# Kernel tuning notes

Measured on AMD Instinct MI355X. Metric: run time of the kernel, lower is better.

Reference implementation:

```python
import jax, jax.numpy as jnp
import numpy as np

N_NODES = 50000
N_EDGES = 640000
D = 128
L = 3


def setup_inputs() -> dict:
    key = jax.random.key(0)
    k1, k2, k3, k4 = jax.random.split(key, 4)
    x = jax.random.normal(k1, (N_NODES, D), dtype=jnp.float32)
    # Glorot-ish scale so activations stay O(1) across 3 layers
    Ws = jax.random.normal(k2, (L, D, D), dtype=jnp.float32) * (1.0 / np.sqrt(D))
    bs = jnp.zeros((L, D), dtype=jnp.float32)
    edge_src = jax.random.randint(k3, (N_EDGES,), 0, N_NODES, dtype=jnp.int32)
    edge_dst = jax.random.randint(k4, (N_EDGES,), 0, N_NODES, dtype=jnp.int32)
    return {"x": x, "Ws": Ws, "bs": bs, "edge_src": edge_src, "edge_dst": edge_dst}


def reference(x, Ws, bs, edge_src, edge_dst):
    n = x.shape[0]
    ones = jnp.ones(edge_src.shape[0], dtype=x.dtype)
    # degrees, clamped to 1 as in dgl GraphConv(norm='both')
    deg_out = jnp.maximum(jax.ops.segment_sum(ones, edge_src, num_segments=n), 1.0)
    deg_in = jnp.maximum(jax.ops.segment_sum(ones, edge_dst, num_segments=n), 1.0)
    inv_sqrt_out = jax.lax.rsqrt(deg_out)[:, None]  # [N,1]
    inv_sqrt_in = jax.lax.rsqrt(deg_in)[:, None]    # [N,1]
    for l in range(Ws.shape[0]):
        h = x * inv_sqrt_out                         # src normalization
        msg = h[edge_src]                            # [E,D] gather
        agg = jax.ops.segment_sum(msg, edge_dst, num_segments=n)  # [N,D] scatter-add
        h = agg * inv_sqrt_in                        # dst normalization
        x = jax.nn.relu(h @ Ws[l] + bs[l])           # linear + ReLU
    return x
```

## Files before the change

kernel.cpp:

```cpp
#include <hip/hip_runtime.h>
#include <hip/hip_fp16.h>

typedef __attribute__((ext_vector_type(8))) _Float16 half8;
typedef __attribute__((ext_vector_type(4))) float f32x4;
typedef unsigned int u32;
typedef unsigned short u16;

#define ELL_PAD 64
#define NCHUNK 64
#define RSZ 8192


__global__ __launch_bounds__(256) void hist2(const int* __restrict__ esrc,
                                             const int* __restrict__ edst,
                                             u32* __restrict__ psrc,
                                             u32* __restrict__ pdst,
                                             const float* __restrict__ Ws,
                                             _Float16* __restrict__ Whi,
                                             _Float16* __restrict__ Wlo,
                                             int E, int N, int chunk, int R,
                                             int histBlocks, int packTotal) {
  __shared__ u32 bs_[RSZ];
  __shared__ u32 bd_[RSZ];
  if (blockIdx.x >= histBlocks) {
    int i = (blockIdx.x - histBlocks) * 256 + threadIdx.x;
    if (i < packTotal) {
      int lane  = i & 63;
      int kstep = (i >> 6) & 3;
      int ntile = (i >> 8) & 7;
      int layer = i >> 11;
      int n  = ntile * 16 + (lane & 15);
      int k0 = kstep * 32 + (lane >> 4) * 8;
      const float* W = Ws + (size_t)layer * 128 * 128;
      size_t base = (size_t)i * 8;
      for (int j = 0; j < 8; j++) {
        float v = W[(k0 + j) * 128 + n];
        _Float16 hi = (_Float16)v;
        Whi[base + j] = hi;
        Wlo[base + j] = (_Float16)(v - (float)hi);
      }
    }
    return;
  }
  int c = blockIdx.x / R;
  int r = blockIdx.x % R;
  int base = r * RSZ;
  int hi = min(RSZ, N - base);
  if (hi <= 0) return;
  for (int j = threadIdx.x; j < RSZ; j += 256) { bs_[j] = 0; bd_[j] = 0; }
  __syncthreads();
  int e0 = c * chunk;
  int e1 = min(E, e0 + chunk);
  for (int i = e0 + threadIdx.x; i < e1; i += 256) {
    unsigned ls = (unsigned)(esrc[i] - base);
    unsigned ld = (unsigned)(edst[i] - base);
    if (ls < (unsigned)RSZ) atomicAdd(&bs_[ls], 1u);
    if (ld < (unsigned)RSZ) atomicAdd(&bd_[ld], 1u);
  }
  __syncthreads();
  u32* ds = psrc + (size_t)c * N + base;
  u32* dd = pdst + (size_t)c * N + base;
  for (int j = threadIdx.x; j < hi; j += 256) { ds[j] = bs_[j]; dd[j] = bd_[j]; }
}


__global__ __launch_bounds__(256) void prep(const u32* __restrict__ psrc,
                                            u32* __restrict__ pdst,
                                            int* __restrict__ deg_out,
                                            int* __restrict__ deg_in, int N) {
  int i = blockIdx.x * 256 + threadIdx.x;
  if (i >= N) return;
  u32 s0 = 0, s1 = 0, s2 = 0, s3 = 0;
#pragma unroll
  for (int c = 0; c < NCHUNK; c += 4) {
    s0 += psrc[(size_t)(c + 0) * N + i];
    s1 += psrc[(size_t)(c + 1) * N + i];
    s2 += psrc[(size_t)(c + 2) * N + i];
    s3 += psrc[(size_t)(c + 3) * N + i];
  }
  deg_out[i] = (int)(s0 + s1 + s2 + s3);
  u32 cnt[NCHUNK];
#pragma unroll
  for (int c = 0; c < NCHUNK; c++) cnt[c] = pdst[(size_t)c * N + i];
  u32 run = (u32)i * ELL_PAD;
#pragma unroll
  for (int c = 0; c < NCHUNK; c++) { u32 t = cnt[c]; cnt[c] = run; run += t; }
#pragma unroll
  for (int c = 0; c < NCHUNK; c++) pdst[(size_t)c * N + i] = cnt[c];
  deg_in[i] = (int)(run - (u32)i * ELL_PAD);
}


__global__ __launch_bounds__(256) void xscale(const float* __restrict__ x,
                                              const int* __restrict__ deg_out,
                                              __half2* __restrict__ xh, int n64) {
  int gid = blockIdx.x * 256 + threadIdx.x;
  if (gid >= n64) return;
  int row = gid >> 6;
  int d = deg_out[row]; if (d < 1) d = 1;
  float s = rsqrtf((float)d);
  float2 v = ((const float2*)x)[gid];
  xh[gid] = __floats2half2_rn(v.x * s, v.y * s);
}


__global__ __launch_bounds__(256) void place(const int* __restrict__ esrc,
                                             const int* __restrict__ edst,
                                             const u32* __restrict__ pdst,
                                             u16* __restrict__ ell,
                                             int E, int N, int chunk, int R) {
  __shared__ u32 cur[RSZ];
  int c = blockIdx.x / R;
  int r = blockIdx.x % R;
  int base = r * RSZ;
  int hi = min(RSZ, N - base);
  if (hi <= 0) return;
  for (int j = threadIdx.x; j < hi; j += 256)
    cur[j] = pdst[(size_t)c * N + base + j];
  __syncthreads();
  int e0 = c * chunk;
  int e1 = min(E, e0 + chunk);
  for (int i = e0 + threadIdx.x; i < e1; i += 256) {
    int d = edst[i];
    unsigned loc = (unsigned)(d - base);
    if (loc < (unsigned)hi) {
      u32 p = atomicAdd(&cur[loc], 1u);
      u32 idx = p - (u32)d * ELL_PAD;
      if (idx < ELL_PAD) ell[p] = (u16)esrc[i];
    }
  }
}


__global__ __launch_bounds__(512) void layer16(const __half2* __restrict__ xh,
                                               const int* __restrict__ deg_in,
                                               const u16* __restrict__ ell,
                                               const _Float16* __restrict__ Whi,
                                               const _Float16* __restrict__ Wlo,
                                               const float* __restrict__ bias,
                                               const int* __restrict__ deg_out,
                                               __half* __restrict__ out16,
                                               float* __restrict__ out32, int n) {
  __shared__ _Float16 As[16 * 136];
  const int wave = threadIdx.x >> 6;
  const int lane = threadIdx.x & 63;
  const int rowBase = blockIdx.x * 16;

  {
    int r0 = rowBase + wave * 2, r1 = r0 + 1;
    int d0 = (r0 < n) ? deg_in[r0] : 0;
    int d1 = (r1 < n) ? deg_in[r1] : 0;
    int l0 = d0 > ELL_PAD ? ELL_PAD : d0;
    int l1 = d1 > ELL_PAD ? ELL_PAD : d1;
    const u16* ep0 = ell + (size_t)(r0 < n ? r0 : 0) * ELL_PAD;
    const u16* ep1 = ell + (size_t)(r1 < n ? r1 : 0) * ELL_PAD;
    float ax0 = 0.f, ay0 = 0.f, ax1 = 0.f, ay1 = 0.f;

    int m = (l0 < l1 ? l0 : l1) & ~3;
    int e = 0;
    for (; e < m; e += 4) {
      ushort4 ia = *(const ushort4*)&ep0[e];
      ushort4 ib = *(const ushort4*)&ep1[e];
      __half2 a0 = xh[(size_t)ia.x * 64 + lane];
      __half2 a1 = xh[(size_t)ia.y * 64 + lane];
      __half2 a2 = xh[(size_t)ia.z * 64 + lane];
      __half2 a3 = xh[(size_t)ia.w * 64 + lane];
      __half2 b0 = xh[(size_t)ib.x * 64 + lane];
      __half2 b1 = xh[(size_t)ib.y * 64 + lane];
      __half2 b2 = xh[(size_t)ib.z * 64 + lane];
      __half2 b3 = xh[(size_t)ib.w * 64 + lane];
      float2 u0 = __half22float2(a0), u1 = __half22float2(a1);
      float2 u2 = __half22float2(a2), u3 = __half22float2(a3);
      float2 w0 = __half22float2(b0), w1 = __half22float2(b1);
      float2 w2 = __half22float2(b2), w3 = __half22float2(b3);
      ax0 += (u0.x + u1.x) + (u2.x + u3.x);
      ay0 += (u0.y + u1.y) + (u2.y + u3.y);
      ax1 += (w0.x + w1.x) + (w2.x + w3.x);
      ay1 += (w0.y + w1.y) + (w2.y + w3.y);
    }
    int e0i = e;
    for (; e0i + 4 <= l0; e0i += 4) {
      ushort4 ia = *(const ushort4*)&ep0[e0i];
      __half2 a0 = xh[(size_t)ia.x * 64 + lane];
      __half2 a1 = xh[(size_t)ia.y * 64 + lane];
      __half2 a2 = xh[(size_t)ia.z * 64 + lane];
      __half2 a3 = xh[(size_t)ia.w * 64 + lane];
      float2 u0 = __half22float2(a0), u1 = __half22float2(a1);
      float2 u2 = __half22float2(a2), u3 = __half22float2(a3);
      ax0 += (u0.x + u1.x) + (u2.x + u3.x);
      ay0 += (u0.y + u1.y) + (u2.y + u3.y);
    }
    for (; e0i < l0; e0i++) {
      float2 v = __half22float2(xh[(size_t)ep0[e0i] * 64 + lane]);
      ax0 += v.x; ay0 += v.y;
    }
    int e1i = e;
    for (; e1i + 4 <= l1; e1i += 4) {
      ushort4 ib = *(const ushort4*)&ep1[e1i];
      __half2 b0 = xh[(size_t)ib.x * 64 + lane];
      __half2 b1 = xh[(size_t)ib.y * 64 + lane];
      __half2 b2 = xh[(size_t)ib.z * 64 + lane];
      __half2 b3 = xh[(size_t)ib.w * 64 + lane];
      float2 w0 = __half22float2(b0), w1 = __half22float2(b1);
      float2 w2 = __half22float2(b2), w3 = __half22float2(b3);
      ax1 += (w0.x + w1.x) + (w2.x + w3.x);
      ay1 += (w0.y + w1.y) + (w2.y + w3.y);
    }
    for (; e1i < l1; e1i++) {
      float2 v = __half22float2(xh[(size_t)ep1[e1i] * 64 + lane]);
      ax1 += v.x; ay1 += v.y;
    }

    float si0 = rsqrtf((float)(d0 < 1 ? 1 : d0));
    float si1 = rsqrtf((float)(d1 < 1 ? 1 : d1));
    *(__half2*)&As[(size_t)(wave * 2 + 0) * 136 + lane * 2] =
        __floats2half2_rn(ax0 * si0, ay0 * si0);
    *(__half2*)&As[(size_t)(wave * 2 + 1) * 136 + lane * 2] =
        __floats2half2_rn(ax1 * si1, ay1 * si1);
  }
  __syncthreads();

  const int quad = lane >> 4;
  const int l16  = lane & 15;
  f32x4 acc = (f32x4){0.f, 0.f, 0.f, 0.f};
#pragma unroll
  for (int ks = 0; ks < 4; ks++) {
    half8 a = *(const half8*)&As[(size_t)l16 * 136 + ks * 32 + quad * 8];
    half8 bh = *(const half8*)&Whi[((wave * 4 + ks) * 64 + lane) * 8];
    half8 bl = *(const half8*)&Wlo[((wave * 4 + ks) * 64 + lane) * 8];
    acc = __builtin_amdgcn_mfma_f32_16x16x32_f16(a, bh, acc, 0, 0, 0);
    acc = __builtin_amdgcn_mfma_f32_16x16x32_f16(a, bl, acc, 0, 0, 0);
  }

  const int r0 = rowBase + quad * 4;
  const int col = wave * 16 + l16;
  const float bv = bias[col];
#pragma unroll
  for (int r = 0; r < 4; r++) {
    int row = r0 + r;
    if (row < n) {
      float v = fmaxf(acc[r] + bv, 0.f);
      if (out16) {
        int d = deg_out[row]; if (d < 1) d = 1;
        out16[(size_t)row * 128 + col] = __float2half(v * rsqrtf((float)d));
      } else {
        out32[(size_t)row * 128 + col] = v;
      }
    }
  }
}


extern "C" void kernel_launch(void* const* d_in, const int* in_sizes, int n_in,
                              void* d_out, int out_size, void* d_ws, size_t ws_size,
                              hipStream_t stream) {
  const float* x   = (const float*)d_in[0];
  const float* Ws  = (const float*)d_in[1];
  const float* bs  = (const float*)d_in[2];
  const int* esrc  = (const int*)d_in[3];
  const int* edst  = (const int*)d_in[4];

  const int D = 128;
  const int N = in_sizes[0] / D;
  const int E = in_sizes[3];
  const int L = in_sizes[1] / (D * D);
  const int Npad = ((N + 15) / 16) * 16;
  const int chunk = (E + NCHUNK - 1) / NCHUNK;
  const int R = (N + RSZ - 1) / RSZ;
  const int histBlocks = NCHUNK * R;
  const int packTotal = L * 2048;
  const int packBlocks = (packTotal + 255) / 256;

  char* base = (char*)d_ws;
  size_t off = 0;
  auto alloc = [&](size_t bytes) {
    char* p = base + off;
    off = (off + bytes + 255) & ~(size_t)255;
    return p;
  };
  int*      deg_out = (int*)alloc((size_t)N * 4);
  int*      deg_in  = (int*)alloc((size_t)N * 4);
  u16*      ell     = (u16*)alloc((size_t)N * ELL_PAD * 2);
  _Float16* Whi     = (_Float16*)alloc((size_t)L * 16384 * 2);
  _Float16* Wlo     = (_Float16*)alloc((size_t)L * 16384 * 2);
  _Float16* xh0     = (_Float16*)alloc((size_t)Npad * 128 * 2);
  _Float16* xh1     = (_Float16*)alloc((size_t)Npad * 128 * 2);
  u32*      psrc    = (u32*)alloc((size_t)NCHUNK * N * 4);
  u32*      pdst    = (u32*)alloc((size_t)NCHUNK * N * 4);

  hist2<<<dim3(histBlocks + packBlocks), dim3(256), 0, stream>>>(
      esrc, edst, psrc, pdst, Ws, Whi, Wlo, E, N, chunk, R, histBlocks, packTotal);
  prep<<<dim3((N + 255) / 256), dim3(256), 0, stream>>>(psrc, pdst, deg_out, deg_in, N);
  xscale<<<dim3((N * 64 + 255) / 256), dim3(256), 0, stream>>>(
      x, deg_out, (__half2*)xh0, N * 64);
  place<<<dim3(histBlocks), dim3(256), 0, stream>>>(
      esrc, edst, pdst, ell, E, N, chunk, R);

  float* outf = (float*)d_out;
  _Float16* ping[2] = {xh0, xh1};
  const dim3 lgrid(Npad / 16), lblk(512);

  for (int l = 0; l < L; l++) {
    bool last = (l == L - 1);
    layer16<<<lgrid, lblk, 0, stream>>>(
        (const __half2*)ping[l & 1], deg_in, ell,
        Whi + (size_t)l * 16384, Wlo + (size_t)l * 16384,
        bs + (size_t)l * D, deg_out,
        last ? nullptr : (__half*)ping[(l + 1) & 1],
        last ? outf : nullptr, N);
  }
}
```

Measured before the change: 263.7 us.

## Fuse degree prep with x scaling and halve edge-chunk count

Merges the prep (degree reduction plus per-chunk prefix offsets) and xscale kernels into one launch. Each node's chunk scan is now split across 4 threads that combine partial sums through shared memory, and NCHUNK drops from 64 to 32, which shrinks the partial-count arrays and the per-thread register array. The goal is to cut a kernel launch and the reduction traffic in preprocessing. The cost is fewer histogram/place blocks with more edges each, so more per-block atomic contention.

```diff
diff --git a/kernel.cpp b/kernel.cpp
--- a/kernel.cpp
+++ b/kernel.cpp
@@ -7,7 +7,7 @@
 typedef unsigned short u16;
 
 #define ELL_PAD 64
-#define NCHUNK 64
+#define NCHUNK 32
 #define RSZ 8192
 
 
@@ -67,40 +67,61 @@
 __global__ __launch_bounds__(256) void prep(const u32* __restrict__ psrc,
                                             u32* __restrict__ pdst,
                                             int* __restrict__ deg_out,
-                                            int* __restrict__ deg_in, int N) {
-  int i = blockIdx.x * 256 + threadIdx.x;
-  if (i >= N) return;
-  u32 s0 = 0, s1 = 0, s2 = 0, s3 = 0;
-#pragma unroll
-  for (int c = 0; c < NCHUNK; c += 4) {
-    s0 += psrc[(size_t)(c + 0) * N + i];
-    s1 += psrc[(size_t)(c + 1) * N + i];
-    s2 += psrc[(size_t)(c + 2) * N + i];
-    s3 += psrc[(size_t)(c + 3) * N + i];
-  }
-  deg_out[i] = (int)(s0 + s1 + s2 + s3);
-  u32 cnt[NCHUNK];
-#pragma unroll
-  for (int c = 0; c < NCHUNK; c++) cnt[c] = pdst[(size_t)c * N + i];
-  u32 run = (u32)i * ELL_PAD;
-#pragma unroll
-  for (int c = 0; c < NCHUNK; c++) { u32 t = cnt[c]; cnt[c] = run; run += t; }
-#pragma unroll
-  for (int c = 0; c < NCHUNK; c++) pdst[(size_t)c * N + i] = cnt[c];
-  deg_in[i] = (int)(run - (u32)i * ELL_PAD);
-}
-
-
-__global__ __launch_bounds__(256) void xscale(const float* __restrict__ x,
-                                              const int* __restrict__ deg_out,
-                                              __half2* __restrict__ xh, int n64) {
-  int gid = blockIdx.x * 256 + threadIdx.x;
-  if (gid >= n64) return;
-  int row = gid >> 6;
-  int d = deg_out[row]; if (d < 1) d = 1;
-  float s = rsqrtf((float)d);
-  float2 v = ((const float2*)x)[gid];
-  xh[gid] = __floats2half2_rn(v.x * s, v.y * s);
+                                            int* __restrict__ deg_in,
+                                            const float* __restrict__ x,
+                                            __half2* __restrict__ xh, int N) {
+  __shared__ u32 sd[64][4];
+  __shared__ u32 ss[64][4];
+  __shared__ float rsL[64];
+  const int tid = threadIdx.x;
+  const int nloc = tid >> 2, p = tid & 3;
+  const int i = blockIdx.x * 64 + nloc;
+
+  u32 cnt[8];
+  u32 sum_d = 0, sum_s = 0;
+  if (i < N) {
+#pragma unroll
+    for (int k = 0; k < 8; k++) {
+      int c = p * 8 + k;
+      cnt[k] = pdst[(size_t)c * N + i];
+      sum_d += cnt[k];
+      sum_s += psrc[(size_t)c * N + i];
+    }
+  }
+  sd[nloc][p] = sum_d;
+  ss[nloc][p] = sum_s;
+  __syncthreads();
+  if (i < N) {
+    u32 run = (u32)i * ELL_PAD;
+#pragma unroll
+    for (int q = 0; q < 4; q++) if (q < p) run += sd[nloc][q];
+#pragma unroll
+    for (int k = 0; k < 8; k++) {
+      u32 t = cnt[k];
+      pdst[(size_t)(p * 8 + k) * N + i] = run;
+      run += t;
+    }
+    if (p == 0) {
+      u32 din  = sd[nloc][0] + sd[nloc][1] + sd[nloc][2] + sd[nloc][3];
+      u32 dout = ss[nloc][0] + ss[nloc][1] + ss[nloc][2] + ss[nloc][3];
+      deg_in[i]  = (int)din;
+      deg_out[i] = (int)dout;
+      rsL[nloc] = rsqrtf((float)(dout < 1 ? 1u : dout));
+    }
+  }
+  __syncthreads();
+  const int row0 = blockIdx.x * 64;
+#pragma unroll
+  for (int k = 0; k < 16; k++) {
+    int j = k * 256 + tid;
+    int lr = j >> 6, col = j & 63;
+    int row = row0 + lr;
+    if (row < N) {
+      float2 v = ((const float2*)x)[(size_t)row * 64 + col];
+      float s = rsL[lr];
+      xh[(size_t)row * 64 + col] = __floats2half2_rn(v.x * s, v.y * s);
+    }
+  }
 }
 
 
@@ -290,9 +311,8 @@
 
   hist2<<<dim3(histBlocks + packBlocks), dim3(256), 0, stream>>>(
       esrc, edst, psrc, pdst, Ws, Whi, Wlo, E, N, chunk, R, histBlocks, packTotal);
-  prep<<<dim3((N + 255) / 256), dim3(256), 0, stream>>>(psrc, pdst, deg_out, deg_in, N);
-  xscale<<<dim3((N * 64 + 255) / 256), dim3(256), 0, stream>>>(
-      x, deg_out, (__half2*)xh0, N * 64);
+  prep<<<dim3((N + 63) / 64), dim3(256), 0, stream>>>(
+      psrc, pdst, deg_out, deg_in, x, (__half2*)xh0, N);
   place<<<dim3(histBlocks), dim3(256), 0, stream>>>(
       esrc, edst, pdst, ell, E, N, chunk, R);
 
```

Result: slower. 292.9 us (+11.1%).
